# Kernel optimization log

Hardware: AMD Instinct MI355X
Metric: run time of the kernel (lower is better)

The kernel has to match this reference:

```python
import jax, jax.numpy as jnp
import numpy as np

N = 100000   # nodes
E = 3200000  # edges (avg degree 32)
G = 1024     # graphs in batch
H = 16       # hidden_dim


def setup_inputs() -> dict:
    key = jax.random.key(0)
    ks = jax.random.split(key, 12)
    p = lambda k, s: jax.random.normal(k, s, dtype=jnp.float32) * 0.1
    return {
        "types": jax.random.randint(ks[0], (N,), 0, 3),
        "pos": jax.random.randint(ks[1], (N,), 0, 3),
        "edge_index": jax.random.randint(ks[2], (2, E), 0, N),
        "batch": jnp.sort(jax.random.randint(ks[3], (N,), 0, G)),
        "W1": p(ks[4], (3, H)), "b1": jnp.zeros((H,), jnp.float32),
        "W2": p(ks[5], (3, H)), "b2": jnp.zeros((H,), jnp.float32),
        "Wg0": p(ks[6], (2 * H, H)), "bg0": jnp.zeros((H,), jnp.float32),
        "Wg1": p(ks[7], (H, H)), "bg1": jnp.zeros((H,), jnp.float32),
        "Wg2": p(ks[8], (H, H)), "bg2": jnp.zeros((H,), jnp.float32),
        "Wo": p(ks[9], (H, 1)), "bo": jnp.zeros((1,), jnp.float32),
    }


def reference(types, pos, edge_index, batch, W1, b1, W2, b2,
              Wg0, bg0, Wg1, bg1, Wg2, bg2, Wo, bo):
    # one-hot encode + linear embed
    xt = jax.nn.one_hot(types, 3, dtype=jnp.float32) @ W1 + b1   # [N, H]
    xp = jax.nn.one_hot(pos, 3, dtype=jnp.float32) @ W2 + b2     # [N, H]
    z = jnp.concatenate([xt, xp], axis=-1)                        # [N, 2H]

    src, dst = edge_index[0], edge_index[1]
    # GCN symmetric normalization with self-loops (gcn_norm)
    deg = jax.ops.segment_sum(jnp.ones((E,), jnp.float32), dst, num_segments=N) + 1.0
    dis = jax.lax.rsqrt(deg)                                      # D^{-1/2}
    edge_coef = (dis[src] * dis[dst])[:, None]                    # [E, 1]
    self_coef = (dis * dis)[:, None]                              # [N, 1]

    def gcn_conv(x, W, b):
        h = x @ W                                                 # [N, H]
        agg = jax.ops.segment_sum(h[src] * edge_coef, dst, num_segments=N)
        return agg + h * self_coef + b

    z = jax.nn.relu(gcn_conv(z, Wg0, bg0))  # dropout=0.2 is train-only; eval mode
    z = jax.nn.relu(gcn_conv(z, Wg1, bg1))
    z = gcn_conv(z, Wg2, bg2)               # no act after last layer

    # global_mean_pool over graph ids
    cnt = jax.ops.segment_sum(jnp.ones((N,), jnp.float32), batch, num_segments=G)
    pooled = jax.ops.segment_sum(z, batch, num_segments=G) / jnp.maximum(cnt, 1.0)[:, None]
    return pooled @ Wo + bo                                       # [G, 1]
```

## Files before the change

### kernel.cpp

```cpp
#include <hip/hip_runtime.h>
#include <hip/hip_fp16.h>

#define NN 100000
#define NE 3200000
#define NG 1024
#define NP 100352
#define NBUCK 391
#define NBLK 256
#define CHUNK ((NE + NBLK - 1) / NBLK)
#define WINCAP 12288

static __device__ inline void acc_u2(float4& acc, uint2 u) {
    __half2* ph = reinterpret_cast<__half2*>(&u);
    float2 lo = __half22float2(ph[0]);
    float2 hi = __half22float2(ph[1]);
    acc.x += lo.x; acc.y += lo.y; acc.z += hi.x; acc.w += hi.y;
}
static __device__ inline uint2 pack4(float a, float b, float c, float d) {
    __half2 lo = __floats2half2_rn(a, b);
    __half2 hi = __floats2half2_rn(c, d);
    uint2 u;
    u.x = *reinterpret_cast<unsigned int*>(&lo);
    u.y = *reinterpret_cast<unsigned int*>(&hi);
    return u;
}
static __device__ inline float4 shfl_xor4(float4 v, int m) {
    float4 r;
    r.x = __shfl_xor(v.x, m); r.y = __shfl_xor(v.y, m);
    r.z = __shfl_xor(v.z, m); r.w = __shfl_xor(v.w, m);
    return r;
}

__global__ void hist_buckets(const int* __restrict__ dst, int* __restrict__ bcnt) {
    __shared__ int sm[NBUCK];
    int tid = threadIdx.x;
    for (int i = tid; i < NBUCK; i += 256) sm[i] = 0;
    __syncthreads();
    int s = blockIdx.x * CHUNK, e = min(NE, s + CHUNK);
    for (int i = s + tid; i < e; i += 256) atomicAdd(&sm[dst[i] >> 8], 1);
    __syncthreads();
    for (int i = tid; i < NBUCK; i += 256)
        if (sm[i]) atomicAdd(&bcnt[i], sm[i]);
}

__global__ void scan_buckets(const int* __restrict__ bcnt, int* __restrict__ bbase) {
    __shared__ int tmp[512];
    int tid = threadIdx.x;
    int v = (tid < NBUCK) ? bcnt[tid] : 0;
    tmp[tid] = v;
    __syncthreads();
    for (int off = 1; off < 512; off <<= 1) {
        int t = (tid >= off) ? tmp[tid - off] : 0;
        __syncthreads();
        tmp[tid] += t;
        __syncthreads();
    }
    if (tid < NBUCK) bbase[tid] = tmp[tid] - v;
}

__global__ void partition(const int* __restrict__ src, const int* __restrict__ dst,
                          const int* __restrict__ bbase, int* __restrict__ bfill,
                          int* __restrict__ part) {
    __shared__ int smh[NBUCK];
    __shared__ int smc[NBUCK];
    int tid = threadIdx.x;
    for (int i = tid; i < NBUCK; i += 256) smh[i] = 0;
    __syncthreads();
    int s = blockIdx.x * CHUNK, e = min(NE, s + CHUNK);
    for (int i = s + tid; i < e; i += 256) atomicAdd(&smh[dst[i] >> 8], 1);
    __syncthreads();
    for (int i = tid; i < NBUCK; i += 256) {
        int c = smh[i];
        smc[i] = c ? (bbase[i] + atomicAdd(&bfill[i], c)) : 0;
    }
    __syncthreads();
    for (int i = s + tid; i < e; i += 256) {
        int d = dst[i];
        int b = d >> 8;
        int p = atomicAdd(&smc[b], 1);
        part[p] = src[i] | ((d & 255) << 17);
    }
}

__global__ void build_csr(const int* __restrict__ part, const int* __restrict__ bbase,
                          const int* __restrict__ bcnt, int* __restrict__ cnt,
                          int* __restrict__ offs, float* __restrict__ dis,
                          int* __restrict__ srcs) {
    __shared__ int sm_cnt[256];
    __shared__ int sm_off[256];
    __shared__ int sm_cur[256];
    __shared__ int sm_win[WINCAP];
    int b = blockIdx.x, tid = threadIdx.x;
    int base = bbase[b], m = bcnt[b];
    sm_cnt[tid] = 0;
    __syncthreads();
    for (int i = tid; i < m; i += 256) atomicAdd(&sm_cnt[part[base + i] >> 17], 1);
    __syncthreads();
    int v = sm_cnt[tid];
    sm_off[tid] = v;
    __syncthreads();
    for (int off = 1; off < 256; off <<= 1) {
        int t = (tid >= off) ? sm_off[tid - off] : 0;
        __syncthreads();
        sm_off[tid] += t;
        __syncthreads();
    }
    int excl = sm_off[tid] - v;
    int n = b * 256 + tid;
    if (n < NN) {
        cnt[n] = v;
        offs[n] = base + excl;
        dis[n] = rsqrtf((float)v + 1.0f);
    }
    sm_cur[tid] = excl;
    __syncthreads();
    if (m <= WINCAP) {
        for (int i = tid; i < m; i += 256) {
            int p = part[base + i];
            int l = atomicAdd(&sm_cur[p >> 17], 1);
            sm_win[l] = p & 0x1FFFF;
        }
        __syncthreads();
        for (int i = tid; i < m; i += 256) srcs[base + i] = sm_win[i];
    } else {
        for (int i = tid; i < m; i += 256) {
            int p = part[base + i];
            int l = atomicAdd(&sm_cur[p >> 17], 1);
            srcs[base + l] = p & 0x1FFFF;
        }
    }
}

__global__ void embed_tf0(const int* __restrict__ types, const int* __restrict__ pos,
                          const float* __restrict__ W1, const float* __restrict__ b1,
                          const float* __restrict__ W2, const float* __restrict__ b2,
                          const float* __restrict__ Wg0, const float* __restrict__ dis,
                          uint2* __restrict__ hs) {
    __shared__ float sW[32 * 16];
    int tid = threadIdx.x;
    sW[tid] = Wg0[tid];
    sW[tid + 256] = Wg0[tid + 256];
    __syncthreads();
    int n = blockIdx.x * 256 + tid;
    if (n >= NN) return;
    int ty = types[n], pp = pos[n];
    float z[32];
#pragma unroll
    for (int j = 0; j < 16; j++) z[j] = W1[ty * 16 + j] + b1[j];
#pragma unroll
    for (int j = 0; j < 16; j++) z[16 + j] = W2[pp * 16 + j] + b2[j];
    float dn = dis[n];
    uint2 o[4];
#pragma unroll
    for (int q = 0; q < 4; q++) {
        float hv[4];
#pragma unroll
        for (int m = 0; m < 4; m++) {
            float a = 0.0f;
#pragma unroll
            for (int k = 0; k < 32; k++) a += z[k] * sW[k * 16 + q * 4 + m];
            hv[m] = a * dn;
        }
        o[q] = pack4(hv[0], hv[1], hv[2], hv[3]);
    }
#pragma unroll
    for (int q = 0; q < 4; q++) hs[(size_t)n * 4 + q] = o[q];
}

template <int RELU, int FUSE_POOL>
__global__ void agg_tf(const uint2* __restrict__ hs, const int* __restrict__ srcs,
                       const int* __restrict__ offs, const int* __restrict__ cnt,
                       const float* __restrict__ dis, const float* __restrict__ bias,
                       const float* __restrict__ Wn, uint2* __restrict__ hs_out,
                       const int* __restrict__ batch,
                       float* __restrict__ pool, int* __restrict__ gcnt) {
    __shared__ float sW[256];
    int tid = threadIdx.x;
    if (!FUSE_POOL) {
        sW[tid] = Wn[tid];
        __syncthreads();
    }
    int gid = blockIdx.x * 256 + tid;
    int n = gid >> 3;
    int q = gid & 3;
    int c = (gid >> 2) & 1;
    if (n >= NN) return;
    int beg = offs[n], deg = cnt[n];
    float dn = dis[n];
    int half = deg >> 1;
    int i = c ? half : 0;
    int iend = c ? deg : half;
    float4 acc = make_float4(0.f, 0.f, 0.f, 0.f);
    for (; i + 8 <= iend; i += 8) {
        int s0 = srcs[beg + i + 0];
        int s1 = srcs[beg + i + 1];
        int s2 = srcs[beg + i + 2];
        int s3 = srcs[beg + i + 3];
        int s4 = srcs[beg + i + 4];
        int s5 = srcs[beg + i + 5];
        int s6 = srcs[beg + i + 6];
        int s7 = srcs[beg + i + 7];
        uint2 a0 = hs[(size_t)s0 * 4 + q];
        uint2 a1 = hs[(size_t)s1 * 4 + q];
        uint2 a2 = hs[(size_t)s2 * 4 + q];
        uint2 a3 = hs[(size_t)s3 * 4 + q];
        uint2 a4 = hs[(size_t)s4 * 4 + q];
        uint2 a5 = hs[(size_t)s5 * 4 + q];
        uint2 a6 = hs[(size_t)s6 * 4 + q];
        uint2 a7 = hs[(size_t)s7 * 4 + q];
        acc_u2(acc, a0); acc_u2(acc, a1); acc_u2(acc, a2); acc_u2(acc, a3);
        acc_u2(acc, a4); acc_u2(acc, a5); acc_u2(acc, a6); acc_u2(acc, a7);
    }
    for (; i < iend; i++) {
        int s = srcs[beg + i];
        acc_u2(acc, hs[(size_t)s * 4 + q]);
    }
    acc.x += __shfl_xor(acc.x, 4);
    acc.y += __shfl_xor(acc.y, 4);
    acc.z += __shfl_xor(acc.z, 4);
    acc.w += __shfl_xor(acc.w, 4);
    if (c != 0) return;
    acc_u2(acc, hs[(size_t)n * 4 + q]);
    float4 b4 = ((const float4*)bias)[q];
    acc.x = fmaf(acc.x, dn, b4.x);
    acc.y = fmaf(acc.y, dn, b4.y);
    acc.z = fmaf(acc.z, dn, b4.z);
    acc.w = fmaf(acc.w, dn, b4.w);
    if (RELU) {
        acc.x = fmaxf(acc.x, 0.f); acc.y = fmaxf(acc.y, 0.f);
        acc.z = fmaxf(acc.z, 0.f); acc.w = fmaxf(acc.w, 0.f);
    }
    if (FUSE_POOL) {
        float4 w4 = ((const float4*)Wn)[q];
        float s = acc.x * w4.x + acc.y * w4.y + acc.z * w4.z + acc.w * w4.w;
        s += __shfl_xor(s, 1);
        s += __shfl_xor(s, 2);
        if (q == 0) {
            int g = batch[n];
            atomicAdd(&pool[g], s);
            atomicAdd(&gcnt[g], 1);
        }
    } else {
        float4 vals[4];
        vals[0] = acc;
        vals[1] = shfl_xor4(acc, 1);
        vals[2] = shfl_xor4(acc, 2);
        vals[3] = shfl_xor4(acc, 3);
        const float4* sW4 = (const float4*)sW;
        float4 hv = make_float4(0.f, 0.f, 0.f, 0.f);
#pragma unroll
        for (int m = 0; m < 4; m++) {
            float4 v = vals[m];
            int rb = (q ^ m) << 2;
            float4 w;
            w = sW4[(rb + 0) * 4 + q];
            hv.x += v.x * w.x; hv.y += v.x * w.y; hv.z += v.x * w.z; hv.w += v.x * w.w;
            w = sW4[(rb + 1) * 4 + q];
            hv.x += v.y * w.x; hv.y += v.y * w.y; hv.z += v.y * w.z; hv.w += v.y * w.w;
            w = sW4[(rb + 2) * 4 + q];
            hv.x += v.z * w.x; hv.y += v.z * w.y; hv.z += v.z * w.z; hv.w += v.z * w.w;
            w = sW4[(rb + 3) * 4 + q];
            hv.x += v.w * w.x; hv.y += v.w * w.y; hv.z += v.w * w.z; hv.w += v.w * w.w;
        }
        hs_out[(size_t)n * 4 + q] = pack4(hv.x * dn, hv.y * dn, hv.z * dn, hv.w * dn);
    }
}

__global__ void finalize(const float* __restrict__ pool, const int* __restrict__ gcnt,
                         const float* __restrict__ bo, float* __restrict__ out) {
    int g = blockIdx.x * 256 + threadIdx.x;
    if (g < NG) {
        float c = fmaxf((float)gcnt[g], 1.0f);
        out[g] = pool[g] / c + bo[0];
    }
}

extern "C" void kernel_launch(void* const* d_in, const int* in_sizes, int n_in,
                              void* d_out, int out_size, void* d_ws, size_t ws_size,
                              hipStream_t stream) {
    const int*   types = (const int*)d_in[0];
    const int*   pos   = (const int*)d_in[1];
    const int*   ei    = (const int*)d_in[2];
    const int*   batch = (const int*)d_in[3];
    const float* W1  = (const float*)d_in[4];
    const float* b1  = (const float*)d_in[5];
    const float* W2  = (const float*)d_in[6];
    const float* b2  = (const float*)d_in[7];
    const float* Wg0 = (const float*)d_in[8];
    const float* bg0 = (const float*)d_in[9];
    const float* Wg1 = (const float*)d_in[10];
    const float* bg1 = (const float*)d_in[11];
    const float* Wg2 = (const float*)d_in[12];
    const float* bg2 = (const float*)d_in[13];
    const float* Wo  = (const float*)d_in[14];
    const float* bo  = (const float*)d_in[15];
    float* out = (float*)d_out;

    const int* esrc = ei;
    const int* edst = ei + NE;

    int*   bcnt  = (int*)d_ws;
    int*   bfill = bcnt + 512;
    float* pool  = (float*)(bfill + 512);
    int*   gcnt  = (int*)(pool + NG);
    int*   bbase = gcnt + NG;
    int*   cnt   = bbase + 512;
    int*   offs  = cnt + NP;
    float* dis   = (float*)(offs + NP);
    int*   srcs  = (int*)(dis + NP);
    int*   part  = srcs + NE;
    uint2* hsA   = (uint2*)part;
    uint2* hsB   = (uint2*)(part + NE / 2);
    (void)ws_size; (void)n_in; (void)in_sizes; (void)out_size;

    hipMemsetAsync(d_ws, 0, (size_t)(1024 + 2 * NG) * sizeof(int), stream);

    const int NB256 = (NN + 255) / 256;
    const int QB8 = (NN * 8 + 255) / 256;

    hist_buckets<<<NBLK, 256, 0, stream>>>(edst, bcnt);
    scan_buckets<<<1, 512, 0, stream>>>(bcnt, bbase);
    partition<<<NBLK, 256, 0, stream>>>(esrc, edst, bbase, bfill, part);
    build_csr<<<NBUCK, 256, 0, stream>>>(part, bbase, bcnt, cnt, offs, dis, srcs);

    embed_tf0<<<NB256, 256, 0, stream>>>(types, pos, W1, b1, W2, b2, Wg0, dis, hsA);
    agg_tf<1, 0><<<QB8, 256, 0, stream>>>(hsA, srcs, offs, cnt, dis, bg0, Wg1, hsB,
                                          batch, pool, gcnt);
    agg_tf<1, 0><<<QB8, 256, 0, stream>>>(hsB, srcs, offs, cnt, dis, bg1, Wg2, hsA,
                                          batch, pool, gcnt);
    agg_tf<0, 1><<<QB8, 256, 0, stream>>>(hsA, srcs, offs, cnt, dis, bg2, Wo, hsB ,
                                          batch, pool, gcnt);

    finalize<<<(NG + 255) / 256, 256, 0, stream>>>(pool, gcnt, bo, out);
}
```

Before: 337.2 us.

## Batch neighbor gathers with padded sentinel row and nontemporal streaming loads

Replaces the 8-way unrolled gather plus scalar tail in the aggregation kernel with 32-wide batches. Out-of-range slots are redirected to a zeroed padding row at index NN, so every batch issues all its loads at once with no tail loop. Streaming reads of edge and partition arrays in the CSR build kernels become nontemporal loads, and launch bounds are added to the aggregation kernel. This trades more registers and wasted loads on short neighbor lists for more memory parallelism, and it needs two extra memsets to clear the padding rows.

After: 365.0 us. 1.08x slower.

```diff
diff --git a/kernel.cpp b/kernel.cpp
--- a/kernel.cpp
+++ b/kernel.cpp
@@ -9,6 +9,7 @@
 #define NBLK 256
 #define CHUNK ((NE + NBLK - 1) / NBLK)
 #define WINCAP 12288
+#define BATCH 32
 
 static __device__ inline void acc_u2(float4& acc, uint2 u) {
     __half2* ph = reinterpret_cast<__half2*>(&u);
@@ -37,7 +38,8 @@
     for (int i = tid; i < NBUCK; i += 256) sm[i] = 0;
     __syncthreads();
     int s = blockIdx.x * CHUNK, e = min(NE, s + CHUNK);
-    for (int i = s + tid; i < e; i += 256) atomicAdd(&sm[dst[i] >> 8], 1);
+    for (int i = s + tid; i < e; i += 256)
+        atomicAdd(&sm[__builtin_nontemporal_load(&dst[i]) >> 8], 1);
     __syncthreads();
     for (int i = tid; i < NBUCK; i += 256)
         if (sm[i]) atomicAdd(&bcnt[i], sm[i]);
@@ -67,7 +69,8 @@
     for (int i = tid; i < NBUCK; i += 256) smh[i] = 0;
     __syncthreads();
     int s = blockIdx.x * CHUNK, e = min(NE, s + CHUNK);
-    for (int i = s + tid; i < e; i += 256) atomicAdd(&smh[dst[i] >> 8], 1);
+    for (int i = s + tid; i < e; i += 256)
+        atomicAdd(&smh[__builtin_nontemporal_load(&dst[i]) >> 8], 1);
     __syncthreads();
     for (int i = tid; i < NBUCK; i += 256) {
         int c = smh[i];
@@ -75,10 +78,11 @@
     }
     __syncthreads();
     for (int i = s + tid; i < e; i += 256) {
-        int d = dst[i];
+        int d = __builtin_nontemporal_load(&dst[i]);
+        int sv = __builtin_nontemporal_load(&src[i]);
         int b = d >> 8;
         int p = atomicAdd(&smc[b], 1);
-        part[p] = src[i] | ((d & 255) << 17);
+        part[p] = sv | ((d & 255) << 17);
     }
 }
 
@@ -94,7 +98,8 @@
     int base = bbase[b], m = bcnt[b];
     sm_cnt[tid] = 0;
     __syncthreads();
-    for (int i = tid; i < m; i += 256) atomicAdd(&sm_cnt[part[base + i] >> 17], 1);
+    for (int i = tid; i < m; i += 256)
+        atomicAdd(&sm_cnt[__builtin_nontemporal_load(&part[base + i]) >> 17], 1);
     __syncthreads();
     int v = sm_cnt[tid];
     sm_off[tid] = v;
@@ -116,7 +121,7 @@
     __syncthreads();
     if (m <= WINCAP) {
         for (int i = tid; i < m; i += 256) {
-            int p = part[base + i];
+            int p = __builtin_nontemporal_load(&part[base + i]);
             int l = atomicAdd(&sm_cur[p >> 17], 1);
             sm_win[l] = p & 0x1FFFF;
         }
@@ -124,7 +129,7 @@
         for (int i = tid; i < m; i += 256) srcs[base + i] = sm_win[i];
     } else {
         for (int i = tid; i < m; i += 256) {
-            int p = part[base + i];
+            int p = __builtin_nontemporal_load(&part[base + i]);
             int l = atomicAdd(&sm_cur[p >> 17], 1);
             srcs[base + l] = p & 0x1FFFF;
         }
@@ -168,12 +173,13 @@
 }
 
 template <int RELU, int FUSE_POOL>
-__global__ void agg_tf(const uint2* __restrict__ hs, const int* __restrict__ srcs,
-                       const int* __restrict__ offs, const int* __restrict__ cnt,
-                       const float* __restrict__ dis, const float* __restrict__ bias,
-                       const float* __restrict__ Wn, uint2* __restrict__ hs_out,
-                       const int* __restrict__ batch,
-                       float* __restrict__ pool, int* __restrict__ gcnt) {
+__global__ __launch_bounds__(256, 2)
+void agg_tf(const uint2* __restrict__ hs, const int* __restrict__ srcs,
+            const int* __restrict__ offs, const int* __restrict__ cnt,
+            const float* __restrict__ dis, const float* __restrict__ bias,
+            const float* __restrict__ Wn, uint2* __restrict__ hs_out,
+            const int* __restrict__ batch,
+            float* __restrict__ pool, int* __restrict__ gcnt) {
     __shared__ float sW[256];
     int tid = threadIdx.x;
     if (!FUSE_POOL) {
@@ -188,32 +194,20 @@
     int beg = offs[n], deg = cnt[n];
     float dn = dis[n];
     int half = deg >> 1;
-    int i = c ? half : 0;
+    int i0 = c ? half : 0;
     int iend = c ? deg : half;
     float4 acc = make_float4(0.f, 0.f, 0.f, 0.f);
-    for (; i + 8 <= iend; i += 8) {
-        int s0 = srcs[beg + i + 0];
-        int s1 = srcs[beg + i + 1];
-        int s2 = srcs[beg + i + 2];
-        int s3 = srcs[beg + i + 3];
-        int s4 = srcs[beg + i + 4];
-        int s5 = srcs[beg + i + 5];
-        int s6 = srcs[beg + i + 6];
-        int s7 = srcs[beg + i + 7];
-        uint2 a0 = hs[(size_t)s0 * 4 + q];
-        uint2 a1 = hs[(size_t)s1 * 4 + q];
-        uint2 a2 = hs[(size_t)s2 * 4 + q];
-        uint2 a3 = hs[(size_t)s3 * 4 + q];
-        uint2 a4 = hs[(size_t)s4 * 4 + q];
-        uint2 a5 = hs[(size_t)s5 * 4 + q];
-        uint2 a6 = hs[(size_t)s6 * 4 + q];
-        uint2 a7 = hs[(size_t)s7 * 4 + q];
-        acc_u2(acc, a0); acc_u2(acc, a1); acc_u2(acc, a2); acc_u2(acc, a3);
-        acc_u2(acc, a4); acc_u2(acc, a5); acc_u2(acc, a6); acc_u2(acc, a7);
-    }
-    for (; i < iend; i++) {
-        int s = srcs[beg + i];
-        acc_u2(acc, hs[(size_t)s * 4 + q]);
+    for (int i = i0; i < iend; i += BATCH) {
+        uint2 a[BATCH];
+#pragma unroll
+        for (int j = 0; j < BATCH; j++) {
+            int idx = i + j;
+            int s = __builtin_nontemporal_load(&srcs[beg + idx]);
+            s = (idx < iend) ? s : NN;
+            a[j] = hs[(size_t)s * 4 + q];
+        }
+#pragma unroll
+        for (int j = 0; j < BATCH; j++) acc_u2(acc, a[j]);
     }
     acc.x += __shfl_xor(acc.x, 4);
     acc.y += __shfl_xor(acc.y, 4);
@@ -323,6 +317,9 @@
     partition<<<NBLK, 256, 0, stream>>>(esrc, edst, bbase, bfill, part);
     build_csr<<<NBUCK, 256, 0, stream>>>(part, bbase, bcnt, cnt, offs, dis, srcs);
 
+    hipMemsetAsync((char*)hsA + (size_t)NN * 32, 0, (size_t)(NP - NN) * 32, stream);
+    hipMemsetAsync((char*)hsB + (size_t)NN * 32, 0, (size_t)(NP - NN) * 32, stream);
+
     embed_tf0<<<NB256, 256, 0, stream>>>(types, pos, W1, b1, W2, b2, Wg0, dis, hsA);
     agg_tf<1, 0><<<QB8, 256, 0, stream>>>(hsA, srcs, offs, cnt, dis, bg0, Wg1, hsB,
                                           batch, pool, gcnt);
```
